# Kernel tuning notes

Hardware: AMD Instinct MI355X
Metric: run time of the kernel (lower is better)

Reference implementation:

```python
import jax, jax.numpy as jnp
import numpy as np

NEG_SLOPE = 0.2

def gat_conv(x, W, a_src, a_dst, b, src, dst, n_nodes):
    # x: [N, F_in], W: [F_in, F_out], a_src/a_dst: [F_out], b: [F_out]
    h = x @ W                                   # [N, F_out]
    alpha_s = h @ a_src                         # [N]
    alpha_d = h @ a_dst                         # [N]
    e = jax.nn.leaky_relu(alpha_s[src] + alpha_d[dst], NEG_SLOPE)  # [E]
    # scatter-softmax over incoming edges of each dst node
    m = jax.ops.segment_max(e, dst, num_segments=n_nodes)
    m = jnp.where(jnp.isfinite(m), m, 0.0)      # nodes with no in-edges
    p = jnp.exp(e - m[dst])
    denom = jax.ops.segment_sum(p, dst, num_segments=n_nodes)
    alpha = p / (denom[dst] + 1e-16)            # [E]
    out = jax.ops.segment_sum(alpha[:, None] * h[src], dst, num_segments=n_nodes)
    return out + b

def setup_inputs() -> dict:
    key = jax.random.key(0)
    N, E, F_IN, H, C = 100000, 1600000, 128, 64, 2
    ks = jax.random.split(key, 10)
    x = jax.random.normal(ks[0], (N, F_IN), dtype=jnp.float32)
    edge_index = jax.random.randint(ks[1], (2, E), 0, N, dtype=jnp.int64)
    s1 = 1.0 / np.sqrt(F_IN)
    s2 = 1.0 / np.sqrt(H)
    return {
        "x": x,
        "edge_index": edge_index,
        "W1": jax.random.normal(ks[2], (F_IN, H), dtype=jnp.float32) * s1,
        "a_src1": jax.random.normal(ks[3], (H,), dtype=jnp.float32) * s2,
        "a_dst1": jax.random.normal(ks[4], (H,), dtype=jnp.float32) * s2,
        "b1": jnp.zeros((H,), dtype=jnp.float32),
        "W2": jax.random.normal(ks[5], (H, C), dtype=jnp.float32) * s2,
        "a_src2": jax.random.normal(ks[6], (C,), dtype=jnp.float32),
        "a_dst2": jax.random.normal(ks[7], (C,), dtype=jnp.float32),
        "b2": jnp.zeros((C,), dtype=jnp.float32),
    }

def reference(x, edge_index, W1, a_src1, a_dst1, b1, W2, a_src2, a_dst2, b2):
    N = x.shape[0]
    loops = jnp.arange(N, dtype=edge_index.dtype)   # GATConv add_self_loops=True
    src = jnp.concatenate([edge_index[0], loops])
    dst = jnp.concatenate([edge_index[1], loops])
    h = gat_conv(x, W1, a_src1, a_dst1, b1, src, dst, N)
    h = jax.nn.relu(h)
    # F.dropout with training=False is identity (eval mode)
    out = gat_conv(h, W2, a_src2, a_dst2, b2, src, dst, N)
    return out
```

## Files before the change

kernel.cpp:

```cpp
#include <hip/hip_runtime.h>
#include <math.h>

constexpr int N_NODES = 100000;
constexpr int N_EDGES = 1600000;
constexpr int F_IN    = 128;
constexpr int F_H     = 64;
constexpr float NEG_SLOPE = 0.2f;

constexpr int NBUCK  = (N_NODES + 255) / 256;
constexpr int BUFCAP = 6144;
constexpr int LCAP   = 6144;
constexpr int CPAD   = 16;

constexpr int SB   = 256;
constexpr int EPT  = 4;
constexpr int EPR  = 256 * EPT;
constexpr int G    = 16;
constexpr int BCAP = 48;

__device__ inline float lrelu(float v) { return v > 0.f ? v : NEG_SLOPE * v; }
__device__ inline float blo(unsigned u) { return __uint_as_float(u << 16); }
__device__ inline float bhi(unsigned u) { return __uint_as_float(u & 0xFFFF0000u); }
__device__ inline unsigned bf16hi(float f) {
    unsigned u = __float_as_uint(f);
    return (u + 0x7FFFu + ((u >> 16) & 1u)) & 0xFFFF0000u;
}
__device__ inline unsigned bf16lo(float f) {
    unsigned u = __float_as_uint(f);
    return (u + 0x7FFFu + ((u >> 16) & 1u)) >> 16;
}

__global__ __launch_bounds__(256) void k_gemm1(
    const float* __restrict__ x, const float* __restrict__ W1,
    const float* __restrict__ a_s, const float* __restrict__ a_d,
    unsigned* __restrict__ h1b, float* __restrict__ as1, float* __restrict__ ad1)
{
    __shared__ float vsP[4][64];
    __shared__ float vdP[4][64];

    const int lane = threadIdx.x & 63;
    const int w    = __builtin_amdgcn_readfirstlane(threadIdx.x >> 6);
    const int fo   = w * 16;
    const int row  = blockIdx.x * 64 + lane;
    const bool valid = row < N_NODES;

    float acc[16];
#pragma unroll
    for (int i = 0; i < 16; ++i) acc[i] = 0.f;

    if (valid) {
        const float4* __restrict__ xr = (const float4*)(x + (size_t)row * F_IN);
        for (int k4 = 0; k4 < F_IN / 4; ++k4) {
            const float4 xv = xr[k4];
            const float* __restrict__ wk = W1 + (size_t)k4 * 4 * F_H + fo;
#pragma unroll
            for (int kk = 0; kk < 4; ++kk) {
                const float xs = (kk == 0) ? xv.x : (kk == 1) ? xv.y : (kk == 2) ? xv.z : xv.w;
                const float* __restrict__ ws = wk + kk * F_H;
#pragma unroll
                for (int i = 0; i < 16; ++i)
                    acc[i] = fmaf(xs, ws[i], acc[i]);
            }
        }
    }

    float vs = 0.f, vd = 0.f;
#pragma unroll
    for (int i = 0; i < 16; ++i) {
        vs = fmaf(acc[i], a_s[fo + i], vs);
        vd = fmaf(acc[i], a_d[fo + i], vd);
    }
    vsP[w][lane] = vs;
    vdP[w][lane] = vd;
    __syncthreads();
    if (w == 0 && valid) {
        as1[row] = vsP[0][lane] + vsP[1][lane] + vsP[2][lane] + vsP[3][lane];
        ad1[row] = vdP[0][lane] + vdP[1][lane] + vdP[2][lane] + vdP[3][lane];
    }

    if (valid) {
        unsigned up[8];
#pragma unroll
        for (int i = 0; i < 8; ++i)
            up[i] = bf16lo(acc[2 * i]) | bf16hi(acc[2 * i + 1]);
        uint4* __restrict__ hr = (uint4*)(h1b + (size_t)row * 32 + w * 8);
        hr[0] = make_uint4(up[0], up[1], up[2], up[3]);
        hr[1] = make_uint4(up[4], up[5], up[6], up[7]);
    }
}

__global__ __launch_bounds__(256) void k_bucketize_staged(
    const int* __restrict__ ei, int* __restrict__ gcur, unsigned* __restrict__ buf)
{
    __shared__ unsigned bin_buf[NBUCK][BCAP];
    __shared__ int bin_cnt[NBUCK];

    const int t = threadIdx.x;
    for (int i = t; i < NBUCK; i += 256) bin_cnt[i] = 0;
    __syncthreads();

    const int per = N_EDGES / SB;
    const int e0 = blockIdx.x * per;
    const int e1 = (blockIdx.x == SB - 1) ? N_EDGES : (e0 + per);

    int cs[EPT], cd[EPT];
#pragma unroll
    for (int q = 0; q < EPT; ++q) {
        const int i = e0 + q * 256 + t;
        cs[q] = (i < e1) ? ei[i] : -1;
        cd[q] = (i < e1) ? ei[N_EDGES + i] : 0;
    }

    for (int base = e0; base < e1; base += EPR) {
        int ls[EPT], ld[EPT];
#pragma unroll
        for (int q = 0; q < EPT; ++q) { ls[q] = cs[q]; ld[q] = cd[q]; }
        const int nbase = base + EPR;
        if (nbase < e1) {
#pragma unroll
            for (int q = 0; q < EPT; ++q) {
                const int i = nbase + q * 256 + t;
                cs[q] = (i < e1) ? ei[i] : -1;
                cd[q] = (i < e1) ? ei[N_EDGES + i] : 0;
            }
        }
#pragma unroll
        for (int q = 0; q < EPT; ++q) {
            if (ls[q] >= 0) {
                const int b = ld[q] >> 8;
                const int pos = atomicAdd(&bin_cnt[b], 1);
                if (pos < BCAP)
                    bin_buf[b][pos] = ((unsigned)ls[q] << 8) | (unsigned)(ld[q] & 255);
            }
        }
        __syncthreads();
        for (int bb = t; bb < NBUCK; bb += 256) {
            const int cnt = bin_cnt[bb];
            if (cnt >= G) {
                const int take = cnt & ~(G - 1);
                const int gbase = atomicAdd(&gcur[bb * CPAD], take);
                if (gbase + take <= BUFCAP) {
                    unsigned* __restrict__ dst = buf + (size_t)bb * BUFCAP + gbase;
                    const int src0 = cnt - take;
                    for (int u = 0; u < take; u += 4) {
                        uint4 v;
                        v.x = bin_buf[bb][src0 + u];
                        v.y = bin_buf[bb][src0 + u + 1];
                        v.z = bin_buf[bb][src0 + u + 2];
                        v.w = bin_buf[bb][src0 + u + 3];
                        *(uint4*)(dst + u) = v;
                    }
                }
                bin_cnt[bb] = cnt - take;
            }
        }
        __syncthreads();
    }
    for (int bb = t; bb < NBUCK; bb += 256) {
        const int cnt = bin_cnt[bb];
        if (cnt > 0) {
            const int gbase = atomicAdd(&gcur[bb * CPAD], cnt);
            if (gbase + cnt <= BUFCAP) {
                unsigned* __restrict__ dst = buf + (size_t)bb * BUFCAP + gbase;
                for (int u = 0; u < cnt; ++u) dst[u] = bin_buf[bb][u];
            }
        }
    }
}

__global__ __launch_bounds__(512) void k_bscan(const int* __restrict__ gcur, int* __restrict__ boff)
{
    __shared__ int sm[512];
    const int t = threadIdx.x;
    const int m = (t < NBUCK) ? min(gcur[t * CPAD], BUFCAP) : 0;
    sm[t] = m;
    __syncthreads();
    for (int o = 1; o < 512; o <<= 1) {
        int a = (t >= o) ? sm[t - o] : 0;
        __syncthreads();
        sm[t] += a;
        __syncthreads();
    }
    if (t < NBUCK) boff[t] = sm[t] - m;
}

__global__ __launch_bounds__(1024) void k_csr_build(
    const int* __restrict__ gcur, const unsigned* __restrict__ buf, const int* __restrict__ boff,
    int* __restrict__ row_start, int* __restrict__ csr)
{
    __shared__ int lcsr[LCAP];
    __shared__ int hist[256];
    __shared__ int lstart[257];
    __shared__ int lcur[256];

    const int b  = blockIdx.x;
    const int t  = threadIdx.x;
    const int nd = min(256, N_NODES - (b << 8));
    const int m  = min(gcur[b * CPAD], BUFCAP);
    const unsigned* __restrict__ sb = buf + (size_t)b * BUFCAP;

    if (t < 256) hist[t] = 0;
    __syncthreads();

    for (int i = t; i < m; i += 1024) atomicAdd(&hist[sb[i] & 255], 1);
    __syncthreads();

    for (int o = 1; o < 256; o <<= 1) {
        int a = 0;
        if (t < 256 && t >= o) a = hist[t - o];
        __syncthreads();
        if (t < 256) hist[t] += a;
        __syncthreads();
    }
    if (t < 256) { lstart[t + 1] = hist[t]; lcur[t] = 0; }
    if (t == 0) lstart[0] = 0;
    __syncthreads();

    for (int i = t; i < m; i += 1024) {
        const unsigned v = sb[i];
        const int dl = v & 255;
        const int p  = atomicAdd(&lcur[dl], 1);
        const int pp = lstart[dl] + p;
        if (pp < LCAP) lcsr[pp] = (int)(v >> 8);
    }
    __syncthreads();

    const int gb   = boff[b];
    const int mtot = lstart[256];
    for (int i = t; i < mtot; i += 1024) csr[gb + i] = lcsr[i];
    if (t < nd) row_start[(b << 8) + t + 1] = gb + lstart[t + 1];
    if (b == 0 && t == 0) row_start[0] = 0;
}

__global__ __launch_bounds__(256) void k_agg1(
    const int* __restrict__ row_start, const int* __restrict__ csr,
    const float* __restrict__ as1, const float* __restrict__ ad1,
    const unsigned* __restrict__ h1b,
    const float* __restrict__ b1, const float* __restrict__ W2,
    const float* __restrict__ a_s2, const float* __restrict__ a_d2,
    float* __restrict__ h2, float* __restrict__ as2, float* __restrict__ ad2)
{
    const int n = blockIdx.x * 4 + (threadIdx.x >> 6);
    const int j = threadIdx.x & 63;
    if (n >= N_NODES) return;

    const int g  = j >> 3;
    const int oq = (j & 7) << 2;

    const int r0  = row_start[n];
    const int deg = row_start[n + 1] - r0;
    const float ad = ad1[n];

    float acc0[8], acc1[8];
#pragma unroll
    for (int i = 0; i < 8; ++i) { acc0[i] = 0.f; acc1[i] = 0.f; }
    float den_l = 0.f;

#define FMA8(ACC, P, U)                                            \
    ACC[0] = fmaf(P, blo(U.x), ACC[0]); ACC[1] = fmaf(P, bhi(U.x), ACC[1]); \
    ACC[2] = fmaf(P, blo(U.y), ACC[2]); ACC[3] = fmaf(P, bhi(U.y), ACC[3]); \
    ACC[4] = fmaf(P, blo(U.z), ACC[4]); ACC[5] = fmaf(P, bhi(U.z), ACC[5]); \
    ACC[6] = fmaf(P, blo(U.w), ACC[6]); ACC[7] = fmaf(P, bhi(U.w), ACC[7]);
#define LD8(S) (*(const uint4*)(h1b + ((size_t)(S) << 5) + oq))

    if (deg <= 63) {
        int sj = n;
        if (j < deg) sj = csr[r0 + j];
        const float aj = as1[sj];
        const int s0 = __shfl(sj, g,      64);
        const int s1 = __shfl(sj, 8 + g,  64);
        const int s2 = __shfl(sj, 16 + g, 64);
        const int s3 = __shfl(sj, 24 + g, 64);
        const uint4 u0 = LD8(s0);
        const uint4 u1 = LD8(s1);
        const uint4 u2 = LD8(s2);
        const uint4 u3 = LD8(s3);
        float pj = 0.f;
        if (j <= deg) pj = __expf(lrelu(aj + ad));
        den_l = pj;
        const float p0 = __shfl(pj, g,      64);
        const float p1 = __shfl(pj, 8 + g,  64);
        const float p2 = __shfl(pj, 16 + g, 64);
        const float p3 = __shfl(pj, 24 + g, 64);
        FMA8(acc0, p0, u0) FMA8(acc1, p1, u1)
        FMA8(acc0, p2, u2) FMA8(acc1, p3, u3)

        const int tot = deg + 1;
        if (tot > 32) {
            const int s4 = __shfl(sj, 32 + g, 64);
            const int s5 = __shfl(sj, 40 + g, 64);
            const int s6 = __shfl(sj, 48 + g, 64);
            const int s7 = __shfl(sj, 56 + g, 64);
            const uint4 u4 = LD8(s4);
            const uint4 u5 = LD8(s5);
            const uint4 u6 = LD8(s6);
            const uint4 u7 = LD8(s7);
            const float p4 = __shfl(pj, 32 + g, 64);
            const float p5 = __shfl(pj, 40 + g, 64);
            const float p6 = __shfl(pj, 48 + g, 64);
            const float p7 = __shfl(pj, 56 + g, 64);
            FMA8(acc0, p4, u4) FMA8(acc1, p5, u5)
            FMA8(acc0, p6, u6) FMA8(acc1, p7, u7)
        }
    } else {
        {
            const float ps = __expf(lrelu(as1[n] + ad));
            if (j == 0) den_l += ps;
            if (g == 0) {
                const uint4 uv = LD8(n);
                FMA8(acc0, ps, uv)
            }
        }
        for (int cb = r0; cb < r0 + deg; cb += 64) {
            const int cnt = min(64, r0 + deg - cb);
            int sj = 0; float pj = 0.f;
            if (j < cnt) { sj = csr[cb + j]; pj = __expf(lrelu(as1[sj] + ad)); }
            den_l += pj;
            for (int base = 0; base < cnt; base += 16) {
                const int   sA = __shfl(sj, base + g, 64);
                const float pA = __shfl(pj, base + g, 64);
                const uint4 ua = LD8(sA);
                FMA8(acc0, pA, ua)
                if (base + 8 < cnt) {
                    const int   sB = __shfl(sj, base + 8 + g, 64);
                    const float pB = __shfl(pj, base + 8 + g, 64);
                    const uint4 ub = LD8(sB);
                    FMA8(acc1, pB, ub)
                }
            }
        }
    }
#undef FMA8
#undef LD8

    float den = den_l;
#pragma unroll
    for (int o = 32; o; o >>= 1) den += __shfl_xor(den, o, 64);

#pragma unroll
    for (int i = 0; i < 8; ++i) acc0[i] += acc1[i];
#pragma unroll
    for (int o = 8; o <= 32; o <<= 1) {
#pragma unroll
        for (int i = 0; i < 8; ++i) acc0[i] += __shfl_xor(acc0[i], o, 64);
    }

    const float inv = 1.f / (den + 1e-16f);
    const int ob = (j & 7) << 3;
    const float4 b0 = *(const float4*)(b1 + ob);
    const float4 b4 = *(const float4*)(b1 + ob + 4);
    float v[8];
    v[0] = acc0[0] * inv + b0.x; v[1] = acc0[1] * inv + b0.y;
    v[2] = acc0[2] * inv + b0.z; v[3] = acc0[3] * inv + b0.w;
    v[4] = acc0[4] * inv + b4.x; v[5] = acc0[5] * inv + b4.y;
    v[6] = acc0[6] * inv + b4.z; v[7] = acc0[7] * inv + b4.w;
#pragma unroll
    for (int i = 0; i < 8; ++i) v[i] = v[i] > 0.f ? v[i] : 0.f;

    const float4* __restrict__ wq = (const float4*)(W2 + 2 * ob);
    const float4 w0 = wq[0], w1 = wq[1], w2 = wq[2], w3 = wq[3];
    float c0 = v[0] * w0.x + v[1] * w0.z + v[2] * w1.x + v[3] * w1.z
             + v[4] * w2.x + v[5] * w2.z + v[6] * w3.x + v[7] * w3.z;
    float c1 = v[0] * w0.y + v[1] * w0.w + v[2] * w1.y + v[3] * w1.w
             + v[4] * w2.y + v[5] * w2.w + v[6] * w3.y + v[7] * w3.w;
#pragma unroll
    for (int o = 1; o <= 4; o <<= 1) {
        c0 += __shfl_xor(c0, o, 64);
        c1 += __shfl_xor(c1, o, 64);
    }
    if (j == 0) {
        h2[n * 2 + 0] = c0;
        h2[n * 2 + 1] = c1;
        as2[n] = c0 * a_s2[0] + c1 * a_s2[1];
        ad2[n] = c0 * a_d2[0] + c1 * a_d2[1];
    }
}

__global__ __launch_bounds__(256) void k_agg2_wave(
    const int* __restrict__ row_start, const int* __restrict__ csr,
    const float* __restrict__ as2, const float* __restrict__ ad2,
    const float* __restrict__ h2, const float* __restrict__ b2,
    float* __restrict__ out)
{
    const int n = blockIdx.x * 4 + (threadIdx.x >> 6);
    const int j = threadIdx.x & 63;
    if (n >= N_NODES) return;
    const int r0  = row_start[n];
    const int deg = row_start[n + 1] - r0;
    const float ad = ad2[n];
    const float2* __restrict__ h22 = (const float2*)h2;

    float den_l = 0.f, x0 = 0.f, x1 = 0.f;
    if (deg <= 63) {
        int sj = n;
        if (j < deg) sj = csr[r0 + j];
        const float  aj = as2[sj];
        const float2 hv = h22[sj];
        float p = 0.f;
        if (j <= deg) p = __expf(lrelu(aj + ad));
        den_l = p; x0 = p * hv.x; x1 = p * hv.y;
    } else {
        if (j == 0) {
            const float p = __expf(lrelu(as2[n] + ad));
            const float2 hv = h22[n];
            den_l = p; x0 = p * hv.x; x1 = p * hv.y;
        }
        for (int idx = r0 + j; idx < r0 + deg; idx += 64) {
            const int s = csr[idx];
            const float p = __expf(lrelu(as2[s] + ad));
            const float2 hv = h22[s];
            den_l += p; x0 = fmaf(p, hv.x, x0); x1 = fmaf(p, hv.y, x1);
        }
    }
#pragma unroll
    for (int o = 32; o; o >>= 1) {
        den_l += __shfl_xor(den_l, o, 64);
        x0    += __shfl_xor(x0, o, 64);
        x1    += __shfl_xor(x1, o, 64);
    }
    if (j == 0) {
        const float inv = 1.f / (den_l + 1e-16f);
        out[n * 2 + 0] = x0 * inv + b2[0];
        out[n * 2 + 1] = x1 * inv + b2[1];
    }
}

extern "C" void kernel_launch(void* const* d_in, const int* in_sizes, int n_in,
                              void* d_out, int out_size, void* d_ws, size_t ws_size,
                              hipStream_t stream)
{
    const float* x    = (const float*)d_in[0];
    const int*   ei   = (const int*)d_in[1];
    const float* W1   = (const float*)d_in[2];
    const float* as1w = (const float*)d_in[3];
    const float* ad1w = (const float*)d_in[4];
    const float* b1   = (const float*)d_in[5];
    const float* W2   = (const float*)d_in[6];
    const float* as2w = (const float*)d_in[7];
    const float* ad2w = (const float*)d_in[8];
    const float* b2   = (const float*)d_in[9];
    float* out = (float*)d_out;

    float* ws = (float*)d_ws;
    size_t off = 0;
    unsigned* h1b = (unsigned*)(ws + off); off += (size_t)N_NODES * 32;
    float* as1 = ws + off; off += N_NODES;
    float* ad1 = ws + off; off += N_NODES;
    float* h2  = ws + off; off += (size_t)N_NODES * 2;
    float* as2 = ws + off; off += N_NODES;
    float* ad2 = ws + off; off += N_NODES;
    int* gcur      = (int*)(ws + off); off += NBUCK * CPAD;
    unsigned* buf  = (unsigned*)(ws + off); off += (size_t)NBUCK * BUFCAP;
    int* boff      = (int*)(ws + off); off += NBUCK + 1;
    int* row_start = (int*)(ws + off); off += N_NODES + 1;
    int* csr       = (int*)(ws + off); off += N_EDGES;

    hipMemsetAsync(gcur, 0, NBUCK * CPAD * sizeof(int), stream);

    k_gemm1           <<<(N_NODES + 63) / 64, 256, 0, stream>>>(x, W1, as1w, ad1w, h1b, as1, ad1);
    k_bucketize_staged<<<SB, 256, 0, stream>>>(ei, gcur, buf);
    k_bscan           <<<1, 512, 0, stream>>>(gcur, boff);
    k_csr_build       <<<NBUCK, 1024, 0, stream>>>(gcur, buf, boff, row_start, csr);
    k_agg1            <<<(N_NODES + 3) / 4, 256, 0, stream>>>(
        row_start, csr, as1, ad1, h1b, b1, W2, as2w, ad2w, h2, as2, ad2);
    k_agg2_wave       <<<(N_NODES + 3) / 4, 256, 0, stream>>>(row_start, csr, as2, ad2, h2, b2, out);
}
```

Before: 246.6 us.

## Slice layer-1 features across XCDs for L2-local gather aggregation

The layer-1 bf16 features are now stored as 8 separate feature slices, each holding 8 bf16 values (16 bytes) per node, instead of 64-byte node rows. Aggregation becomes one block per (32-node group, slice), with 8 threads per node striding over edges. Because the slice index is blockIdx&7, each slice tends to be served by one XCD, so its 1.6MB random-gather working set can stay in that XCD's L2. In exchange, csr and as1 are read and the edge exponentials recomputed 8 times, one per slice. The layer-2 projections are summed across slices with float atomics, which needs an extra memset and makes the summation order nondeterministic.

```diff
diff --git a/kernel.cpp b/kernel.cpp
--- a/kernel.cpp
+++ b/kernel.cpp
@@ -83,9 +83,8 @@
 #pragma unroll
         for (int i = 0; i < 8; ++i)
             up[i] = bf16lo(acc[2 * i]) | bf16hi(acc[2 * i + 1]);
-        uint4* __restrict__ hr = (uint4*)(h1b + (size_t)row * 32 + w * 8);
-        hr[0] = make_uint4(up[0], up[1], up[2], up[3]);
-        hr[1] = make_uint4(up[4], up[5], up[6], up[7]);
+        *(uint4*)(h1b + ((size_t)(2 * w)     * N_NODES + row) * 4) = make_uint4(up[0], up[1], up[2], up[3]);
+        *(uint4*)(h1b + ((size_t)(2 * w + 1) * N_NODES + row) * 4) = make_uint4(up[4], up[5], up[6], up[7]);
     }
 }
 
@@ -232,7 +231,7 @@
     if (b == 0 && t == 0) row_start[0] = 0;
 }
 
-__global__ __launch_bounds__(256) void k_agg1(
+__global__ __launch_bounds__(256) void k_agg1_slice(
     const int* __restrict__ row_start, const int* __restrict__ csr,
     const float* __restrict__ as1, const float* __restrict__ ad1,
     const unsigned* __restrict__ h1b,
@@ -240,139 +239,56 @@
     const float* __restrict__ a_s2, const float* __restrict__ a_d2,
     float* __restrict__ h2, float* __restrict__ as2, float* __restrict__ ad2)
 {
-    const int n = blockIdx.x * 4 + (threadIdx.x >> 6);
-    const int j = threadIdx.x & 63;
-    if (n >= N_NODES) return;
-
-    const int g  = j >> 3;
-    const int oq = (j & 7) << 2;
+    const int s  = blockIdx.x & 7;
+    const int nb = blockIdx.x >> 3;
+    const int t  = threadIdx.x;
+    const int n  = nb * 32 + (t >> 3);
+    const int e  = t & 7;
+    const unsigned* __restrict__ hp = h1b + (size_t)s * N_NODES * 4;
 
     const int r0  = row_start[n];
     const int deg = row_start[n + 1] - r0;
     const float ad = ad1[n];
 
-    float acc0[8], acc1[8];
-#pragma unroll
-    for (int i = 0; i < 8; ++i) { acc0[i] = 0.f; acc1[i] = 0.f; }
-    float den_l = 0.f;
-
-#define FMA8(ACC, P, U)                                            \
-    ACC[0] = fmaf(P, blo(U.x), ACC[0]); ACC[1] = fmaf(P, bhi(U.x), ACC[1]); \
-    ACC[2] = fmaf(P, blo(U.y), ACC[2]); ACC[3] = fmaf(P, bhi(U.y), ACC[3]); \
-    ACC[4] = fmaf(P, blo(U.z), ACC[4]); ACC[5] = fmaf(P, bhi(U.z), ACC[5]); \
-    ACC[6] = fmaf(P, blo(U.w), ACC[6]); ACC[7] = fmaf(P, bhi(U.w), ACC[7]);
-#define LD8(S) (*(const uint4*)(h1b + ((size_t)(S) << 5) + oq))
-
-    if (deg <= 63) {
-        int sj = n;
-        if (j < deg) sj = csr[r0 + j];
-        const float aj = as1[sj];
-        const int s0 = __shfl(sj, g,      64);
-        const int s1 = __shfl(sj, 8 + g,  64);
-        const int s2 = __shfl(sj, 16 + g, 64);
-        const int s3 = __shfl(sj, 24 + g, 64);
-        const uint4 u0 = LD8(s0);
-        const uint4 u1 = LD8(s1);
-        const uint4 u2 = LD8(s2);
-        const uint4 u3 = LD8(s3);
-        float pj = 0.f;
-        if (j <= deg) pj = __expf(lrelu(aj + ad));
-        den_l = pj;
-        const float p0 = __shfl(pj, g,      64);
-        const float p1 = __shfl(pj, 8 + g,  64);
-        const float p2 = __shfl(pj, 16 + g, 64);
-        const float p3 = __shfl(pj, 24 + g, 64);
-        FMA8(acc0, p0, u0) FMA8(acc1, p1, u1)
-        FMA8(acc0, p2, u2) FMA8(acc1, p3, u3)
-
-        const int tot = deg + 1;
-        if (tot > 32) {
-            const int s4 = __shfl(sj, 32 + g, 64);
-            const int s5 = __shfl(sj, 40 + g, 64);
-            const int s6 = __shfl(sj, 48 + g, 64);
-            const int s7 = __shfl(sj, 56 + g, 64);
-            const uint4 u4 = LD8(s4);
-            const uint4 u5 = LD8(s5);
-            const uint4 u6 = LD8(s6);
-            const uint4 u7 = LD8(s7);
-            const float p4 = __shfl(pj, 32 + g, 64);
-            const float p5 = __shfl(pj, 40 + g, 64);
-            const float p6 = __shfl(pj, 48 + g, 64);
-            const float p7 = __shfl(pj, 56 + g, 64);
-            FMA8(acc0, p4, u4) FMA8(acc1, p5, u5)
-            FMA8(acc0, p6, u6) FMA8(acc1, p7, u7)
-        }
-    } else {
-        {
-            const float ps = __expf(lrelu(as1[n] + ad));
-            if (j == 0) den_l += ps;
-            if (g == 0) {
-                const uint4 uv = LD8(n);
-                FMA8(acc0, ps, uv)
-            }
-        }
-        for (int cb = r0; cb < r0 + deg; cb += 64) {
-            const int cnt = min(64, r0 + deg - cb);
-            int sj = 0; float pj = 0.f;
-            if (j < cnt) { sj = csr[cb + j]; pj = __expf(lrelu(as1[sj] + ad)); }
-            den_l += pj;
-            for (int base = 0; base < cnt; base += 16) {
-                const int   sA = __shfl(sj, base + g, 64);
-                const float pA = __shfl(pj, base + g, 64);
-                const uint4 ua = LD8(sA);
-                FMA8(acc0, pA, ua)
-                if (base + 8 < cnt) {
-                    const int   sB = __shfl(sj, base + 8 + g, 64);
-                    const float pB = __shfl(pj, base + 8 + g, 64);
-                    const uint4 ub = LD8(sB);
-                    FMA8(acc1, pB, ub)
-                }
-            }
-        }
-    }
-#undef FMA8
-#undef LD8
-
-    float den = den_l;
-#pragma unroll
-    for (int o = 32; o; o >>= 1) den += __shfl_xor(den, o, 64);
-
-#pragma unroll
-    for (int i = 0; i < 8; ++i) acc0[i] += acc1[i];
-#pragma unroll
-    for (int o = 8; o <= 32; o <<= 1) {
-#pragma unroll
-        for (int i = 0; i < 8; ++i) acc0[i] += __shfl_xor(acc0[i], o, 64);
+    float acc[8];
+#pragma unroll
+    for (int i = 0; i < 8; ++i) acc[i] = 0.f;
+    float den = 0.f;
+
+    for (int slot = e; slot <= deg; slot += 8) {
+        const int sj = (slot < deg) ? csr[r0 + slot] : n;
+        const uint4 u = *(const uint4*)(hp + ((size_t)sj << 2));
+        const float p = __expf(lrelu(as1[sj] + ad));
+        den += p;
+        acc[0] = fmaf(p, blo(u.x), acc[0]); acc[1] = fmaf(p, bhi(u.x), acc[1]);
+        acc[2] = fmaf(p, blo(u.y), acc[2]); acc[3] = fmaf(p, bhi(u.y), acc[3]);
+        acc[4] = fmaf(p, blo(u.z), acc[4]); acc[5] = fmaf(p, bhi(u.z), acc[5]);
+        acc[6] = fmaf(p, blo(u.w), acc[6]); acc[7] = fmaf(p, bhi(u.w), acc[7]);
+    }
+
+#pragma unroll
+    for (int o = 1; o <= 4; o <<= 1) {
+        den += __shfl_xor(den, o, 64);
+#pragma unroll
+        for (int i = 0; i < 8; ++i) acc[i] += __shfl_xor(acc[i], o, 64);
     }
 
     const float inv = 1.f / (den + 1e-16f);
-    const int ob = (j & 7) << 3;
-    const float4 b0 = *(const float4*)(b1 + ob);
-    const float4 b4 = *(const float4*)(b1 + ob + 4);
-    float v[8];
-    v[0] = acc0[0] * inv + b0.x; v[1] = acc0[1] * inv + b0.y;
-    v[2] = acc0[2] * inv + b0.z; v[3] = acc0[3] * inv + b0.w;
-    v[4] = acc0[4] * inv + b4.x; v[5] = acc0[5] * inv + b4.y;
-    v[6] = acc0[6] * inv + b4.z; v[7] = acc0[7] * inv + b4.w;
-#pragma unroll
-    for (int i = 0; i < 8; ++i) v[i] = v[i] > 0.f ? v[i] : 0.f;
-
-    const float4* __restrict__ wq = (const float4*)(W2 + 2 * ob);
-    const float4 w0 = wq[0], w1 = wq[1], w2 = wq[2], w3 = wq[3];
-    float c0 = v[0] * w0.x + v[1] * w0.z + v[2] * w1.x + v[3] * w1.z
-             + v[4] * w2.x + v[5] * w2.z + v[6] * w3.x + v[7] * w3.z;
-    float c1 = v[0] * w0.y + v[1] * w0.w + v[2] * w1.y + v[3] * w1.w
-             + v[4] * w2.y + v[5] * w2.w + v[6] * w3.y + v[7] * w3.w;
+    const int f = s * 8 + e;
+    float v = acc[e] * inv + b1[f];
+    v = v > 0.f ? v : 0.f;
+    float c0 = v * W2[2 * f + 0];
+    float c1 = v * W2[2 * f + 1];
 #pragma unroll
     for (int o = 1; o <= 4; o <<= 1) {
         c0 += __shfl_xor(c0, o, 64);
         c1 += __shfl_xor(c1, o, 64);
     }
-    if (j == 0) {
-        h2[n * 2 + 0] = c0;
-        h2[n * 2 + 1] = c1;
-        as2[n] = c0 * a_s2[0] + c1 * a_s2[1];
-        ad2[n] = c0 * a_d2[0] + c1 * a_d2[1];
+    if (e == 0) {
+        atomicAdd(&h2[2 * n + 0], c0);
+        atomicAdd(&h2[2 * n + 1], c1);
+        atomicAdd(&as2[n], c0 * a_s2[0] + c1 * a_s2[1]);
+        atomicAdd(&ad2[n], c0 * a_d2[0] + c1 * a_d2[1]);
     }
 }
 
@@ -456,12 +372,13 @@
     int* csr       = (int*)(ws + off); off += N_EDGES;
 
     hipMemsetAsync(gcur, 0, NBUCK * CPAD * sizeof(int), stream);
+    hipMemsetAsync(h2, 0, (size_t)N_NODES * 4 * sizeof(float), stream);
 
     k_gemm1           <<<(N_NODES + 63) / 64, 256, 0, stream>>>(x, W1, as1w, ad1w, h1b, as1, ad1);
     k_bucketize_staged<<<SB, 256, 0, stream>>>(ei, gcur, buf);
     k_bscan           <<<1, 512, 0, stream>>>(gcur, boff);
     k_csr_build       <<<NBUCK, 1024, 0, stream>>>(gcur, buf, boff, row_start, csr);
-    k_agg1            <<<(N_NODES + 3) / 4, 256, 0, stream>>>(
+    k_agg1_slice      <<<(N_NODES / 32) * 8, 256, 0, stream>>>(
         row_start, csr, as1, ad1, h1b, b1, W2, as2w, ad2w, h2, as2, ad2);
     k_agg2_wave       <<<(N_NODES + 3) / 4, 256, 0, stream>>>(row_start, csr, as2, ad2, h2, b2, out);
 }
```

Result: slower. 315.4 us (+27.9%).
